# Kernel optimization log

Hardware: AMD Instinct MI355X
Metric: run time of the kernel (lower is better)

## Reference

```python
import jax, jax.numpy as jnp
import numpy as np

B, S, H, A = 16, 2048, 1024, 1024


def setup_inputs() -> dict:
    key = jax.random.key(0)
    k1, k2, k3 = jax.random.split(key, 3)
    x = jax.random.normal(k1, (B, S, H), dtype=jnp.float32)
    # learned params (nn.Parameter tensors in the torch module)
    w_a = jax.random.normal(k2, (H, A), dtype=jnp.float32) * 0.02
    query = jax.random.normal(k3, (H, A), dtype=jnp.float32) * 0.02
    return {"x": x, "w_a": w_a, "query": query}


def reference(x, w_a, query):
    # semantic attention: values = x
    key = jnp.tanh(x @ w_a)          # [B, S, A]
    q = x @ query                    # [B, S, A]  (per-token semantic query)
    # temp[b, s, t] = q[b, s] . key[b, t]
    temp = jnp.einsum('bsa,bta->bst', q, key)  # [B, S, S]
    seq_len = x.shape[1]
    # softmax mask: strictly-upper triangle = -inf, lower+diag = 0 (causal)
    causal = jnp.triu(jnp.ones((seq_len, seq_len), dtype=bool), k=1)
    softmax_mask = jnp.where(causal, -jnp.inf, 0.0).astype(x.dtype)
    d = jax.nn.softmax(temp + softmax_mask, axis=-1)  # [B, S, S]
    a = d @ x                        # [B, S, H]
    return (a, d)
```

## Files before the change

### kernel.cpp

```cpp
#include <hip/hip_runtime.h>

typedef _Float16 f16x8 __attribute__((ext_vector_type(8)));
typedef float f32x4 __attribute__((ext_vector_type(4)));
typedef unsigned short u16;
typedef u16 u16x8 __attribute__((ext_vector_type(8)));

#define NBATCH 16
#define NSEQ   2048
#define NHID   1024
#define MALL   (NBATCH * NSEQ)

__device__ __forceinline__ u16 f16_rne(float x) {
    _Float16 h = (_Float16)x;
    return __builtin_bit_cast(u16, h);
}
__device__ __forceinline__ float fast_tanh(float x) {
    float e = __expf(2.0f * x);
    return 1.0f - 2.0f / (e + 1.0f);
}

#define GLOAD16(g, l) __builtin_amdgcn_global_load_lds(                         \
    (const __attribute__((address_space(1))) unsigned int*)(g),                 \
    (__attribute__((address_space(3))) unsigned int*)(l), 16, 0, 0)


#define NOPS ((void)0)
#define VMW4 asm volatile("s_waitcnt vmcnt(4)" ::: "memory");
#define VMW0 asm volatile("s_waitcnt vmcnt(0)" ::: "memory");

#define MMQ(MH, I, J0, J1, J2, J3)                                             \
    MM(acc[MH][0][(I)&3][0], I, J0); MM(acc[MH][0][(I)&3][1], I, J1);          \
    MM(acc[MH][1][(I)&3][0], I, J2); MM(acc[MH][1][(I)&3][1], I, J3);

#define MMBLK_P(MH)                                                            \
    MMQ(MH,0,0,1,2,3) MMQ(MH,1,0,1,2,3) MMQ(MH,2,0,1,2,3) MMQ(MH,3,0,1,2,3)    \
    MMQ(MH,4,4,5,6,7) MMQ(MH,5,4,5,6,7) MMQ(MH,6,4,5,6,7) MMQ(MH,7,4,5,6,7)

#define TILE64(C, ST0, ST1, W) {                                               \
    LDA(0,C,0,0); LDA(1,C,0,0); LDA(2,C,0,0); LDA(3,C,0,0);                    \
    LDA(4,C,0,1); LDA(5,C,0,1); LDA(6,C,0,1); LDA(7,C,0,1);                    \
    LDB(0,C,0,0); LDB(1,C,0,0); LDB(2,C,1,0); LDB(3,C,1,0);                    \
    LDB(4,C,0,1); LDB(5,C,0,1); LDB(6,C,1,1); LDB(7,C,1,1);                    \
    ST0;                                                                       \
    __builtin_amdgcn_s_barrier();                                              \
    asm volatile("s_waitcnt lgkmcnt(0)" ::: "memory");                         \
    __builtin_amdgcn_sched_barrier(0);                                         \
    __builtin_amdgcn_s_setprio(1);                                             \
    MMBLK_P(0)                                                                 \
    __builtin_amdgcn_s_setprio(0);                                             \
    __builtin_amdgcn_s_barrier();                                              \
    LDA(0,C,1,0); LDA(1,C,1,0); LDA(2,C,1,0); LDA(3,C,1,0);                    \
    LDA(4,C,1,1); LDA(5,C,1,1); LDA(6,C,1,1); LDA(7,C,1,1);                    \
    ST1;                                                                       \
    __builtin_amdgcn_s_barrier();                                              \
    asm volatile("s_waitcnt lgkmcnt(0)" ::: "memory");                         \
    __builtin_amdgcn_sched_barrier(0);                                         \
    __builtin_amdgcn_s_setprio(1);                                             \
    MMBLK_P(1)                                                                 \
    __builtin_amdgcn_s_setprio(0);                                             \
    W;                                                                         \
    __builtin_amdgcn_s_barrier();                                              \
}

__device__ __forceinline__ void gemm_core64(
    const u16* __restrict__ Ap, int Arow0,
    const u16* __restrict__ Bp, int Brow0,
    u16* lds, f32x4 (&acc)[2][2][4][2])
{
    int tid = threadIdx.x;
    int l = tid & 63, w = tid >> 6;
    int wr = w >> 2, wc = w & 3;
    int fr = l & 15, sg = l >> 4;

    f16x8 ah[8], bh[8];

    auto LDA = [&](int i, int C, int MH, int KH) {
        int rb = MH * 128 + wr * 64 + (i & 3) * 16 + fr;
        int sl = ((KH * 4 + sg) ^ (rb & 7)) * 8;
        ah[i] = *(const f16x8*)&lds[C * 32768 + rb * 64 + sl];
    };
    auto LDB = [&](int j, int C, int NH, int KH) {
        int rb = NH * 128 + wc * 32 + (j & 1) * 16 + fr;
        int sl = ((KH * 4 + sg) ^ (rb & 7)) * 8;
        bh[j] = *(const f16x8*)&lds[C * 32768 + 16384 + rb * 64 + sl];
    };
    auto MM = [&](f32x4& d, int i, int j) {
        d = __builtin_amdgcn_mfma_f32_16x16x32_f16(ah[i], bh[j], d, 0, 0, 0);
    };
    auto STA = [&](int C, int H, int T) {
        int rg = Arow0 + H * 128 + w * 8 + (l >> 3);
        const u16* s = Ap + (size_t)rg * 1024 + (size_t)T * 64
                       + ((l & 7) ^ (rg & 7)) * 8;
        u16* d = &lds[C * 32768 + (H * 128 + w * 8) * 64];
        GLOAD16(s, d);
        GLOAD16(s + (size_t)64 * 1024, d + 64 * 64);
    };
    auto STB = [&](int C, int H, int T) {
        int rg = Brow0 + H * 128 + w * 8 + (l >> 3);
        const u16* s = Bp + (size_t)rg * 1024 + (size_t)T * 64
                       + ((l & 7) ^ (rg & 7)) * 8;
        u16* d = &lds[C * 32768 + 16384 + (H * 128 + w * 8) * 64];
        GLOAD16(s, d);
        GLOAD16(s + (size_t)64 * 1024, d + 64 * 64);
    };

    STA(0, 0, 0); STA(0, 1, 0); STB(0, 0, 0); STB(0, 1, 0);
    STA(1, 0, 1); STB(1, 0, 1);
    VMW4
    __builtin_amdgcn_s_barrier();

    for (int u = 0; u < 13; u += 2) {
        TILE64(0, (STA(1,1,u+1), STB(1,1,u+1)), (STA(0,0,u+2), STB(0,0,u+2)), VMW4)
        TILE64(1, (STA(0,1,u+2), STB(0,1,u+2)), (STA(1,0,u+3), STB(1,0,u+3)), VMW4)
    }
    TILE64(0, (STA(1,1,15), STB(1,1,15)), NOPS, VMW0)
    TILE64(1, NOPS, NOPS, NOPS)
}

__global__ __launch_bounds__(256) void wprep_kernel(
    const float* __restrict__ wa, const float* __restrict__ qu,
    u16* __restrict__ wT)
{
    int idx = blockIdx.x * 256 + threadIdx.x;
    int h = idx >> 10, n = idx & 1023;
    wT[(size_t)n * 1024 + h]          = f16_rne(wa[idx] * 64.0f);
    wT[(size_t)(1024 + n) * 1024 + h] = f16_rne(qu[idx] * 64.0f);
}

__global__ __launch_bounds__(256) void xprep_kernel(
    const float* __restrict__ x, u16* __restrict__ xT,
    u16* __restrict__ x_f16)
{
    __shared__ u16 tile[64][65];
    int b = blockIdx.z;
    int t0 = blockIdx.x * 64;
    int h0 = blockIdx.y * 64;
    const float* xb = x + (size_t)b * NSEQ * NHID;
    int tid = threadIdx.x;
    #pragma unroll
    for (int i = 0; i < 16; i++) {
        int e = i * 256 + tid;
        int tl = e >> 6, hl = e & 63;
        float v = xb[(size_t)(t0 + tl) * NHID + h0 + hl];
        u16 bv = f16_rne(v);
        tile[tl][hl] = bv;
        x_f16[(size_t)(b * NSEQ + t0 + tl) * NHID + h0 + hl] = bv;
    }
    __syncthreads();
    u16* xTb = xT + (size_t)b * NHID * NSEQ;
    #pragma unroll
    for (int i = 0; i < 16; i++) {
        int e = i * 256 + tid;
        int hl = e >> 6, tl = e & 63;
        xTb[(size_t)(h0 + hl) * NSEQ + t0 + tl] = tile[tl][hl];
    }
}

__global__ __launch_bounds__(512, 2) void k1_gemm(
    const u16* __restrict__ x_f16, const u16* __restrict__ wT,
    u16* __restrict__ k_f16, u16* __restrict__ q_f16)
{
    extern __shared__ u16 lds[];
    int wg = blockIdx.x;
    int nid = (wg & 7) * 128 + (wg >> 3);
    int n0 = (nid & 7) * 256;
    int m0 = (nid >> 3) * 256;
    bool is_key = (n0 < 1024);

    f32x4 acc[2][2][4][2] = {};
    gemm_core64(x_f16, m0, wT, n0, lds, acc);

    int tid = threadIdx.x;
    int l = tid & 63, w = tid >> 6;
    int wr = w >> 2, wc = w & 3;
    int fr = l & 15, fq = l >> 4;
    int nb = is_key ? n0 : (n0 - 1024);
    u16* outp = is_key ? k_f16 : q_f16;
    #pragma unroll
    for (int mh = 0; mh < 2; mh++)
    #pragma unroll
    for (int nh = 0; nh < 2; nh++)
    #pragma unroll
    for (int m = 0; m < 4; m++)
    #pragma unroll
    for (int n = 0; n < 2; n++)
    #pragma unroll
    for (int j = 0; j < 4; j++) {
        int grow = m0 + mh * 128 + wr * 64 + m * 16 + fq * 4 + j;
        int c    = nb + nh * 128 + wc * 32 + n * 16 + fr;
        float v = acc[mh][nh][m][n][j] * 0.015625f;
        outp[(size_t)grow * 1024 + c] = f16_rne(is_key ? fast_tanh(v) : v);
    }
}

__global__ __launch_bounds__(512, 2) void k2_logits(
    const u16* __restrict__ q_f16, const u16* __restrict__ k_f16,
    float* __restrict__ dmat)
{
    extern __shared__ u16 lds[];
    int wg = blockIdx.x;
    int nid = (wg & 7) * 72 + (wg >> 3);
    int b = nid / 36;
    int lin = nid - b * 36;
    int st = 0;
    while ((st + 1) * (st + 2) / 2 <= lin) st++;
    int tt = lin - st * (st + 1) / 2;
    int s0 = st * 256, t0 = tt * 256;
    int base = b * NSEQ;

    f32x4 acc[2][2][4][2] = {};
    gemm_core64(q_f16, base + s0, k_f16, base + t0, lds, acc);

    float* db = dmat + (size_t)b * NSEQ * NSEQ;
    int tid = threadIdx.x;
    int l = tid & 63, w = tid >> 6;
    int wr = w >> 2, wc = w & 3;
    int fr = l & 15, fq = l >> 4;
    #pragma unroll
    for (int mh = 0; mh < 2; mh++)
    #pragma unroll
    for (int nh = 0; nh < 2; nh++)
    #pragma unroll
    for (int m = 0; m < 4; m++)
    #pragma unroll
    for (int n = 0; n < 2; n++)
    #pragma unroll
    for (int j = 0; j < 4; j++) {
        int s = s0 + mh * 128 + wr * 64 + m * 16 + fq * 4 + j;
        int t = t0 + nh * 128 + wc * 32 + n * 16 + fr;
        if (t <= s) db[(size_t)s * NSEQ + t] = acc[mh][nh][m][n][j];
    }
}

__global__ __launch_bounds__(256) void k3_softmax(
    float* __restrict__ dmat, u16* __restrict__ d_f16)
{
    __shared__ float redm[4];
    __shared__ float reds[4];
    int rowid = blockIdx.x;
    int s = rowid & (NSEQ - 1);
    float* row = dmat + (size_t)rowid * NSEQ;
    int tid = threadIdx.x;
    int lane = tid & 63, w = tid >> 6;
    int t0 = tid * 8;

    float v[8];
    if (t0 <= s) {
        float4 a = *(const float4*)&row[t0];
        float4 c = *(const float4*)&row[t0 + 4];
        v[0] = a.x; v[1] = a.y; v[2] = a.z; v[3] = a.w;
        v[4] = c.x; v[5] = c.y; v[6] = c.z; v[7] = c.w;
        #pragma unroll
        for (int i = 0; i < 8; i++) if (t0 + i > s) v[i] = -INFINITY;
    } else {
        #pragma unroll
        for (int i = 0; i < 8; i++) v[i] = -INFINITY;
    }

    float m = -INFINITY;
    #pragma unroll
    for (int i = 0; i < 8; i++) m = fmaxf(m, v[i]);
    #pragma unroll
    for (int off = 32; off > 0; off >>= 1) m = fmaxf(m, __shfl_xor(m, off));
    if (lane == 0) redm[w] = m;
    __syncthreads();
    m = fmaxf(fmaxf(redm[0], redm[1]), fmaxf(redm[2], redm[3]));

    float sum = 0.f;
    float ev[8];
    #pragma unroll
    for (int i = 0; i < 8; i++) {
        ev[i] = (t0 + i <= s) ? __expf(v[i] - m) : 0.f;
        sum += ev[i];
    }
    #pragma unroll
    for (int off = 32; off > 0; off >>= 1) sum += __shfl_xor(sum, off);
    if (lane == 0) reds[w] = sum;
    __syncthreads();
    sum = reds[0] + reds[1] + reds[2] + reds[3];
    float inv = 1.0f / sum;

    float4 o0, o1;
    o0.x = ev[0] * inv; o0.y = ev[1] * inv; o0.z = ev[2] * inv; o0.w = ev[3] * inv;
    o1.x = ev[4] * inv; o1.y = ev[5] * inv; o1.z = ev[6] * inv; o1.w = ev[7] * inv;
    *(float4*)&row[t0] = o0;
    *(float4*)&row[t0 + 4] = o1;
    u16x8 bv;
    bv[0] = f16_rne(o0.x); bv[1] = f16_rne(o0.y); bv[2] = f16_rne(o0.z); bv[3] = f16_rne(o0.w);
    bv[4] = f16_rne(o1.x); bv[5] = f16_rne(o1.y); bv[6] = f16_rne(o1.z); bv[7] = f16_rne(o1.w);
    *(u16x8*)&d_f16[(size_t)rowid * NSEQ + t0] = bv;
}

__global__ __launch_bounds__(256) void k4_av(
    const u16* __restrict__ d_f16,
    const u16* __restrict__ xT,
    float* __restrict__ aout)
{
    __shared__ u16 sa[128 * 32];
    __shared__ u16 sb[128 * 32];

    int wg = blockIdx.x;
    int nid = (wg & 7) * 256 + (wg >> 3);
    int n0 = (nid & 7) * 128;
    int s0 = ((nid >> 3) & 15) * 128;
    int b = nid >> 7;

    int tid = threadIdx.x;
    int lane = tid & 63;
    int w = tid >> 6;
    int wr = w >> 1, wc = w & 1;

    int srow = w * 16 + (lane >> 2);
    int sslot = ((lane & 3) ^ ((lane >> 3) & 3)) * 8;

    const u16* pa = d_f16 + (size_t)(b * NSEQ + s0 + srow) * NSEQ + sslot;
    const u16* pb = xT + ((size_t)b * NHID + n0 + srow) * NSEQ + sslot;
    u16* da0 = &sa[(w * 16) * 32];  u16* da1 = &sa[(64 + w * 16) * 32];
    u16* db0 = &sb[(w * 16) * 32];  u16* db1 = &sb[(64 + w * 16) * 32];
    const size_t R64 = (size_t)64 * NSEQ;

    int fr = lane & 15, sg = lane >> 4;
    int rsl = (sg ^ ((fr >> 1) & 3)) * 8;

    f32x4 acc[4][4] = {};
    int kmax = s0 + 128;

    for (int kk = 0; kk < kmax; kk += 32) {
        __syncthreads();
        GLOAD16(pa + kk, da0); GLOAD16(pa + kk + R64, da1);
        GLOAD16(pb + kk, db0); GLOAD16(pb + kk + R64, db1);
        __syncthreads();

        f16x8 af[4], bf[4];
        #pragma unroll
        for (int m = 0; m < 4; m++)
            af[m] = *(const f16x8*)&sa[(wr * 64 + m * 16 + fr) * 32 + rsl];
        #pragma unroll
        for (int n = 0; n < 4; n++)
            bf[n] = *(const f16x8*)&sb[(wc * 64 + n * 16 + fr) * 32 + rsl];
        #pragma unroll
        for (int m = 0; m < 4; m++)
            #pragma unroll
            for (int n = 0; n < 4; n++)
                acc[m][n] = __builtin_amdgcn_mfma_f32_16x16x32_f16(af[m], bf[n], acc[m][n], 0, 0, 0);
    }

    float* ab = aout + (size_t)b * NSEQ * NHID;
    int fq = lane >> 4;
    #pragma unroll
    for (int m = 0; m < 4; m++)
        #pragma unroll
        for (int n = 0; n < 4; n++)
            #pragma unroll
            for (int j = 0; j < 4; j++) {
                int s = s0 + wr * 64 + m * 16 + fq * 4 + j;
                int h = n0 + wc * 64 + n * 16 + fr;
                ab[(size_t)s * NHID + h] = acc[m][n][j];
            }
}

extern "C" void kernel_launch(void* const* d_in, const int* in_sizes, int n_in,
                              void* d_out, int out_size, void* d_ws, size_t ws_size,
                              hipStream_t stream)
{
    const float* x     = (const float*)d_in[0];
    const float* w_a   = (const float*)d_in[1];
    const float* query = (const float*)d_in[2];

    float* aout = (float*)d_out;
    float* dmat = aout + (size_t)NBATCH * NSEQ * NHID;

    char* p = (char*)d_ws;
    u16* q_f16  = (u16*)p; p += (size_t)MALL * 1024 * 2;
    u16* x_f16  = (u16*)p; p += (size_t)MALL * 1024 * 2;
    u16* k_f16  = (u16*)p; p += (size_t)MALL * 1024 * 2;
    u16* d_f16  = x_f16;
    u16* xT     = (u16*)p; p += (size_t)MALL * 1024 * 2;
    u16* wT     = (u16*)p; p += (size_t)2048 * 1024 * 2;
    (void)ws_size; (void)in_sizes; (void)n_in; (void)out_size;

    hipFuncSetAttribute((const void*)k1_gemm,
                        hipFuncAttributeMaxDynamicSharedMemorySize, 131072);
    hipFuncSetAttribute((const void*)k2_logits,
                        hipFuncAttributeMaxDynamicSharedMemorySize, 131072);

    wprep_kernel<<<dim3(4096), 256, 0, stream>>>(w_a, query, wT);
    xprep_kernel<<<dim3(32, 16, 16), 256, 0, stream>>>(x, xT, x_f16);
    k1_gemm<<<dim3(1024), 512, 131072, stream>>>(x_f16, wT, k_f16, q_f16);
    k2_logits<<<dim3(576), 512, 131072, stream>>>(q_f16, k_f16, dmat);
    k3_softmax<<<dim3(32768), 256, 0, stream>>>(dmat, d_f16);
    k4_av<<<dim3(2048), 256, 0, stream>>>(d_f16, xT, aout);
}
```

Measured before the change: 569.2 us.

## Reuse pipelined 256x256 GEMM core for AV, pipeline LDS reads, vectorize xprep

The causal d@x kernel now uses the shared 256x256-tile, double-buffered GEMM core with a templated stride and a variable tile count, skipping K tiles above the diagonal. Heavy tiles are scheduled first. The GEMM core also splits its LDS fragment reads so the second-half A fragments are loaded early behind a partial lgkmcnt wait, overlapping reads with MFMA. The x transpose/convert kernel switches to float4 loads and 4-wide half stores with a padded tile. Larger tiles give fewer blocks (512) for the AV stage, which may hurt load balance.

```diff
diff --git a/kernel.cpp b/kernel.cpp
--- a/kernel.cpp
+++ b/kernel.cpp
@@ -3,6 +3,7 @@
 typedef _Float16 f16x8 __attribute__((ext_vector_type(8)));
 typedef float f32x4 __attribute__((ext_vector_type(4)));
 typedef unsigned short u16;
+typedef u16 u16x4 __attribute__((ext_vector_type(4)));
 typedef u16 u16x8 __attribute__((ext_vector_type(8)));
 
 #define NBATCH 16
@@ -28,80 +29,94 @@
 #define VMW4 asm volatile("s_waitcnt vmcnt(4)" ::: "memory");
 #define VMW0 asm volatile("s_waitcnt vmcnt(0)" ::: "memory");
 
-#define MMQ(MH, I, J0, J1, J2, J3)                                             \
-    MM(acc[MH][0][(I)&3][0], I, J0); MM(acc[MH][0][(I)&3][1], I, J1);          \
-    MM(acc[MH][1][(I)&3][0], I, J2); MM(acc[MH][1][(I)&3][1], I, J3);
-
-#define MMBLK_P(MH)                                                            \
-    MMQ(MH,0,0,1,2,3) MMQ(MH,1,0,1,2,3) MMQ(MH,2,0,1,2,3) MMQ(MH,3,0,1,2,3)    \
-    MMQ(MH,4,4,5,6,7) MMQ(MH,5,4,5,6,7) MMQ(MH,6,4,5,6,7) MMQ(MH,7,4,5,6,7)
+#define MMQ4(ARR, MH, M, FI, J0, J1, J2, J3)                                   \
+    MMp(acc[MH][0][M][0], ARR[FI], bh[J0]);                                    \
+    MMp(acc[MH][0][M][1], ARR[FI], bh[J1]);                                    \
+    MMp(acc[MH][1][M][0], ARR[FI], bh[J2]);                                    \
+    MMp(acc[MH][1][M][1], ARR[FI], bh[J3]);
 
 #define TILE64(C, ST0, ST1, W) {                                               \
     LDA(0,C,0,0); LDA(1,C,0,0); LDA(2,C,0,0); LDA(3,C,0,0);                    \
     LDA(4,C,0,1); LDA(5,C,0,1); LDA(6,C,0,1); LDA(7,C,0,1);                    \
     LDB(0,C,0,0); LDB(1,C,0,0); LDB(2,C,1,0); LDB(3,C,1,0);                    \
     LDB(4,C,0,1); LDB(5,C,0,1); LDB(6,C,1,1); LDB(7,C,1,1);                    \
+    __builtin_amdgcn_sched_barrier(0);                                         \
+    LDA2(0,C,0); LDA2(1,C,0); LDA2(2,C,0); LDA2(3,C,0);                        \
+    __builtin_amdgcn_sched_barrier(0);                                         \
     ST0;                                                                       \
     __builtin_amdgcn_s_barrier();                                              \
-    asm volatile("s_waitcnt lgkmcnt(0)" ::: "memory");                         \
+    asm volatile("s_waitcnt lgkmcnt(4)" ::: "memory");                         \
     __builtin_amdgcn_sched_barrier(0);                                         \
     __builtin_amdgcn_s_setprio(1);                                             \
-    MMBLK_P(0)                                                                 \
+    MMQ4(ah,0,0,0, 0,1,2,3) MMQ4(ah,0,1,1, 0,1,2,3)                            \
+    MMQ4(ah,0,2,2, 0,1,2,3) MMQ4(ah,0,3,3, 0,1,2,3)                            \
+    MMQ4(ah,0,0,4, 4,5,6,7) MMQ4(ah,0,1,5, 4,5,6,7)                            \
+    MMQ4(ah,0,2,6, 4,5,6,7) MMQ4(ah,0,3,7, 4,5,6,7)                            \
     __builtin_amdgcn_s_setprio(0);                                             \
     __builtin_amdgcn_s_barrier();                                              \
-    LDA(0,C,1,0); LDA(1,C,1,0); LDA(2,C,1,0); LDA(3,C,1,0);                    \
     LDA(4,C,1,1); LDA(5,C,1,1); LDA(6,C,1,1); LDA(7,C,1,1);                    \
+    __builtin_amdgcn_sched_barrier(0);                                         \
     ST1;                                                                       \
-    __builtin_amdgcn_s_barrier();                                              \
+    asm volatile("s_waitcnt lgkmcnt(4)" ::: "memory");                         \
+    __builtin_amdgcn_sched_barrier(0);                                         \
+    __builtin_amdgcn_s_setprio(1);                                             \
+    MMQ4(ah2,1,0,0, 0,1,2,3) MMQ4(ah2,1,1,1, 0,1,2,3)                          \
+    MMQ4(ah2,1,2,2, 0,1,2,3) MMQ4(ah2,1,3,3, 0,1,2,3)                          \
     asm volatile("s_waitcnt lgkmcnt(0)" ::: "memory");                         \
     __builtin_amdgcn_sched_barrier(0);                                         \
-    __builtin_amdgcn_s_setprio(1);                                             \
-    MMBLK_P(1)                                                                 \
+    MMQ4(ah,1,0,4, 4,5,6,7) MMQ4(ah,1,1,5, 4,5,6,7)                            \
+    MMQ4(ah,1,2,6, 4,5,6,7) MMQ4(ah,1,3,7, 4,5,6,7)                            \
     __builtin_amdgcn_s_setprio(0);                                             \
     W;                                                                         \
     __builtin_amdgcn_s_barrier();                                              \
 }
 
+template<int AST, int BST>
 __device__ __forceinline__ void gemm_core64(
     const u16* __restrict__ Ap, int Arow0,
     const u16* __restrict__ Bp, int Brow0,
-    u16* lds, f32x4 (&acc)[2][2][4][2])
+    int nt, u16* lds, f32x4 (&acc)[2][2][4][2])
 {
     int tid = threadIdx.x;
     int l = tid & 63, w = tid >> 6;
     int wr = w >> 2, wc = w & 3;
     int fr = l & 15, sg = l >> 4;
 
-    f16x8 ah[8], bh[8];
+    f16x8 ah[8], ah2[4], bh[8];
 
     auto LDA = [&](int i, int C, int MH, int KH) {
         int rb = MH * 128 + wr * 64 + (i & 3) * 16 + fr;
         int sl = ((KH * 4 + sg) ^ (rb & 7)) * 8;
         ah[i] = *(const f16x8*)&lds[C * 32768 + rb * 64 + sl];
     };
+    auto LDA2 = [&](int i, int C, int KH) {
+        int rb = 128 + wr * 64 + i * 16 + fr;
+        int sl = ((KH * 4 + sg) ^ (rb & 7)) * 8;
+        ah2[i] = *(const f16x8*)&lds[C * 32768 + rb * 64 + sl];
+    };
     auto LDB = [&](int j, int C, int NH, int KH) {
         int rb = NH * 128 + wc * 32 + (j & 1) * 16 + fr;
         int sl = ((KH * 4 + sg) ^ (rb & 7)) * 8;
         bh[j] = *(const f16x8*)&lds[C * 32768 + 16384 + rb * 64 + sl];
     };
-    auto MM = [&](f32x4& d, int i, int j) {
-        d = __builtin_amdgcn_mfma_f32_16x16x32_f16(ah[i], bh[j], d, 0, 0, 0);
+    auto MMp = [&](f32x4& d, f16x8 a, f16x8 b) {
+        d = __builtin_amdgcn_mfma_f32_16x16x32_f16(a, b, d, 0, 0, 0);
     };
     auto STA = [&](int C, int H, int T) {
         int rg = Arow0 + H * 128 + w * 8 + (l >> 3);
-        const u16* s = Ap + (size_t)rg * 1024 + (size_t)T * 64
+        const u16* s = Ap + (size_t)rg * AST + (size_t)T * 64
                        + ((l & 7) ^ (rg & 7)) * 8;
         u16* d = &lds[C * 32768 + (H * 128 + w * 8) * 64];
         GLOAD16(s, d);
-        GLOAD16(s + (size_t)64 * 1024, d + 64 * 64);
+        GLOAD16(s + (size_t)64 * AST, d + 64 * 64);
     };
     auto STB = [&](int C, int H, int T) {
         int rg = Brow0 + H * 128 + w * 8 + (l >> 3);
-        const u16* s = Bp + (size_t)rg * 1024 + (size_t)T * 64
+        const u16* s = Bp + (size_t)rg * BST + (size_t)T * 64
                        + ((l & 7) ^ (rg & 7)) * 8;
         u16* d = &lds[C * 32768 + 16384 + (H * 128 + w * 8) * 64];
         GLOAD16(s, d);
-        GLOAD16(s + (size_t)64 * 1024, d + 64 * 64);
+        GLOAD16(s + (size_t)64 * BST, d + 64 * 64);
     };
 
     STA(0, 0, 0); STA(0, 1, 0); STB(0, 0, 0); STB(0, 1, 0);
@@ -109,11 +124,11 @@
     VMW4
     __builtin_amdgcn_s_barrier();
 
-    for (int u = 0; u < 13; u += 2) {
+    for (int u = 0; u + 2 < nt; u += 2) {
         TILE64(0, (STA(1,1,u+1), STB(1,1,u+1)), (STA(0,0,u+2), STB(0,0,u+2)), VMW4)
         TILE64(1, (STA(0,1,u+2), STB(0,1,u+2)), (STA(1,0,u+3), STB(1,0,u+3)), VMW4)
     }
-    TILE64(0, (STA(1,1,15), STB(1,1,15)), NOPS, VMW0)
+    TILE64(0, (STA(1,1,nt-1), STB(1,1,nt-1)), NOPS, VMW0)
     TILE64(1, NOPS, NOPS, NOPS)
 }
 
@@ -131,28 +146,35 @@
     const float* __restrict__ x, u16* __restrict__ xT,
     u16* __restrict__ x_f16)
 {
-    __shared__ u16 tile[64][65];
+    __shared__ u16 tile[64][68];
     int b = blockIdx.z;
     int t0 = blockIdx.x * 64;
     int h0 = blockIdx.y * 64;
-    const float* xb = x + (size_t)b * NSEQ * NHID;
-    int tid = threadIdx.x;
-    #pragma unroll
-    for (int i = 0; i < 16; i++) {
-        int e = i * 256 + tid;
-        int tl = e >> 6, hl = e & 63;
-        float v = xb[(size_t)(t0 + tl) * NHID + h0 + hl];
-        u16 bv = f16_rne(v);
-        tile[tl][hl] = bv;
-        x_f16[(size_t)(b * NSEQ + t0 + tl) * NHID + h0 + hl] = bv;
+    const float* xb = x + ((size_t)b * NSEQ + t0) * NHID + h0;
+    int tid = threadIdx.x;
+    int tl = tid >> 4;
+    int hl = (tid & 15) * 4;
+    #pragma unroll
+    for (int i = 0; i < 4; i++) {
+        int r = i * 16 + tl;
+        float4 v = *(const float4*)&xb[(size_t)r * NHID + hl];
+        u16x4 hv;
+        hv[0] = f16_rne(v.x); hv[1] = f16_rne(v.y);
+        hv[2] = f16_rne(v.z); hv[3] = f16_rne(v.w);
+        *(u16x4*)&tile[r][hl] = hv;
+        *(u16x4*)&x_f16[((size_t)(b * NSEQ) + t0 + r) * NHID + h0 + hl] = hv;
     }
     __syncthreads();
-    u16* xTb = xT + (size_t)b * NHID * NSEQ;
-    #pragma unroll
-    for (int i = 0; i < 16; i++) {
-        int e = i * 256 + tid;
-        int hl = e >> 6, tl = e & 63;
-        xTb[(size_t)(h0 + hl) * NSEQ + t0 + tl] = tile[tl][hl];
+    u16* xTb = xT + ((size_t)b * NHID + h0) * NSEQ + t0;
+    int hl2 = tid >> 4;
+    int tl2 = (tid & 15) * 4;
+    #pragma unroll
+    for (int i = 0; i < 4; i++) {
+        int hh = i * 16 + hl2;
+        u16x4 o;
+        o[0] = tile[tl2 + 0][hh]; o[1] = tile[tl2 + 1][hh];
+        o[2] = tile[tl2 + 2][hh]; o[3] = tile[tl2 + 3][hh];
+        *(u16x4*)&xTb[(size_t)hh * NSEQ + tl2] = o;
     }
 }
 
@@ -168,7 +190,7 @@
     bool is_key = (n0 < 1024);
 
     f32x4 acc[2][2][4][2] = {};
-    gemm_core64(x_f16, m0, wT, n0, lds, acc);
+    gemm_core64<1024, 1024>(x_f16, m0, wT, n0, 16, lds, acc);
 
     int tid = threadIdx.x;
     int l = tid & 63, w = tid >> 6;
@@ -209,7 +231,7 @@
     int base = b * NSEQ;
 
     f32x4 acc[2][2][4][2] = {};
-    gemm_core64(q_f16, base + s0, k_f16, base + t0, lds, acc);
+    gemm_core64<1024, 1024>(q_f16, base + s0, k_f16, base + t0, 16, lds, acc);
 
     float* db = dmat + (size_t)b * NSEQ * NSEQ;
     int tid = threadIdx.x;
@@ -291,72 +313,44 @@
     *(u16x8*)&d_f16[(size_t)rowid * NSEQ + t0] = bv;
 }
 
-__global__ __launch_bounds__(256) void k4_av(
+__global__ __launch_bounds__(512, 2) void k4_av(
     const u16* __restrict__ d_f16,
     const u16* __restrict__ xT,
     float* __restrict__ aout)
 {
-    __shared__ u16 sa[128 * 32];
-    __shared__ u16 sb[128 * 32];
-
+    extern __shared__ u16 lds[];
     int wg = blockIdx.x;
-    int nid = (wg & 7) * 256 + (wg >> 3);
-    int n0 = (nid & 7) * 128;
-    int s0 = ((nid >> 3) & 15) * 128;
-    int b = nid >> 7;
-
-    int tid = threadIdx.x;
-    int lane = tid & 63;
-    int w = tid >> 6;
-    int wr = w >> 1, wc = w & 1;
-
-    int srow = w * 16 + (lane >> 2);
-    int sslot = ((lane & 3) ^ ((lane >> 3) & 3)) * 8;
-
-    const u16* pa = d_f16 + (size_t)(b * NSEQ + s0 + srow) * NSEQ + sslot;
-    const u16* pb = xT + ((size_t)b * NHID + n0 + srow) * NSEQ + sslot;
-    u16* da0 = &sa[(w * 16) * 32];  u16* da1 = &sa[(64 + w * 16) * 32];
-    u16* db0 = &sb[(w * 16) * 32];  u16* db1 = &sb[(64 + w * 16) * 32];
-    const size_t R64 = (size_t)64 * NSEQ;
-
-    int fr = lane & 15, sg = lane >> 4;
-    int rsl = (sg ^ ((fr >> 1) & 3)) * 8;
-
-    f32x4 acc[4][4] = {};
-    int kmax = s0 + 128;
-
-    for (int kk = 0; kk < kmax; kk += 32) {
-        __syncthreads();
-        GLOAD16(pa + kk, da0); GLOAD16(pa + kk + R64, da1);
-        GLOAD16(pb + kk, db0); GLOAD16(pb + kk + R64, db1);
-        __syncthreads();
-
-        f16x8 af[4], bf[4];
-        #pragma unroll
-        for (int m = 0; m < 4; m++)
-            af[m] = *(const f16x8*)&sa[(wr * 64 + m * 16 + fr) * 32 + rsl];
-        #pragma unroll
-        for (int n = 0; n < 4; n++)
-            bf[n] = *(const f16x8*)&sb[(wc * 64 + n * 16 + fr) * 32 + rsl];
-        #pragma unroll
-        for (int m = 0; m < 4; m++)
-            #pragma unroll
-            for (int n = 0; n < 4; n++)
-                acc[m][n] = __builtin_amdgcn_mfma_f32_16x16x32_f16(af[m], bf[n], acc[m][n], 0, 0, 0);
-    }
+    int nid = (wg & 7) * 64 + (wg >> 3);
+    int b = nid & 15;
+    int rest = nid >> 4;
+    int ntile = rest & 3;
+    int st = 7 - (rest >> 2);
+    int s0 = st * 256;
+    int n0 = ntile * 256;
+    int nt = 4 * (st + 1);
+
+    f32x4 acc[2][2][4][2] = {};
+    gemm_core64<2048, 2048>(d_f16, b * 2048 + s0, xT, b * 1024 + n0, nt, lds, acc);
 
     float* ab = aout + (size_t)b * NSEQ * NHID;
-    int fq = lane >> 4;
+    int tid = threadIdx.x;
+    int l = tid & 63, w = tid >> 6;
+    int wr = w >> 2, wc = w & 3;
+    int fr = l & 15, fq = l >> 4;
+    #pragma unroll
+    for (int mh = 0; mh < 2; mh++)
+    #pragma unroll
+    for (int nh = 0; nh < 2; nh++)
     #pragma unroll
     for (int m = 0; m < 4; m++)
-        #pragma unroll
-        for (int n = 0; n < 4; n++)
-            #pragma unroll
-            for (int j = 0; j < 4; j++) {
-                int s = s0 + wr * 64 + m * 16 + fq * 4 + j;
-                int h = n0 + wc * 64 + n * 16 + fr;
-                ab[(size_t)s * NHID + h] = acc[m][n][j];
-            }
+    #pragma unroll
+    for (int n = 0; n < 2; n++)
+    #pragma unroll
+    for (int j = 0; j < 4; j++) {
+        int s = s0 + mh * 128 + wr * 64 + m * 16 + fq * 4 + j;
+        int c = n0 + nh * 128 + wc * 32 + n * 16 + fr;
+        ab[(size_t)s * NHID + c] = acc[mh][nh][m][n][j];
+    }
 }
 
 extern "C" void kernel_launch(void* const* d_in, const int* in_sizes, int n_in,
@@ -383,11 +377,13 @@
                         hipFuncAttributeMaxDynamicSharedMemorySize, 131072);
     hipFuncSetAttribute((const void*)k2_logits,
                         hipFuncAttributeMaxDynamicSharedMemorySize, 131072);
+    hipFuncSetAttribute((const void*)k4_av,
+                        hipFuncAttributeMaxDynamicSharedMemorySize, 131072);
 
     wprep_kernel<<<dim3(4096), 256, 0, stream>>>(w_a, query, wT);
     xprep_kernel<<<dim3(32, 16, 16), 256, 0, stream>>>(x, xT, x_f16);
     k1_gemm<<<dim3(1024), 512, 131072, stream>>>(x_f16, wT, k_f16, q_f16);
     k2_logits<<<dim3(576), 512, 131072, stream>>>(q_f16, k_f16, dmat);
     k3_softmax<<<dim3(32768), 256, 0, stream>>>(dmat, d_f16);
-    k4_av<<<dim3(2048), 256, 0, stream>>>(d_f16, xT, aout);
-}
+    k4_av<<<dim3(512), 512, 131072, stream>>>(d_f16, xT, aout);
+}
```

After: 682.0 us. +19.8%, slower.
